# Performance work log

Measured on AMD Instinct MI355X. Metric: run time of the kernel, lower is better.

The kernel has to match this reference:

```python
import jax, jax.numpy as jnp
import numpy as np
from jax.ops import segment_sum

N_NODES = 50000
N_EDGES = 800000
IN_CH = 128
HID = 256
N_CLASSES = 10
N_GRAPHS = 64


def setup_inputs() -> dict:
    key = jax.random.key(0)
    ks = jax.random.split(key, 12)
    x = jax.random.normal(ks[0], (N_NODES, IN_CH), dtype=jnp.float32)
    edge_index = jax.random.randint(ks[1], (2, N_EDGES), 0, N_NODES, dtype=jnp.int64)
    batch = jnp.sort(jax.random.randint(ks[2], (N_NODES,), 0, N_GRAPHS, dtype=jnp.int64))
    def glorot(k, shape):
        lim = (6.0 / (shape[0] + shape[1])) ** 0.5
        return jax.random.uniform(k, shape, jnp.float32, -lim, lim)
    # GraphConv has two linear maps: lin_rel (neighbor aggregate, with bias) and lin_root (self)
    params = {
        "W1_root": glorot(ks[3], (IN_CH, HID)),  "W1_nbr": glorot(ks[4], (IN_CH, HID)),  "b1": jnp.zeros((HID,), jnp.float32),
        "W2_root": glorot(ks[5], (HID, HID)),    "W2_nbr": glorot(ks[6], (HID, HID)),    "b2": jnp.zeros((HID,), jnp.float32),
        "W3_root": glorot(ks[7], (HID, HID)),    "W3_nbr": glorot(ks[8], (HID, HID)),    "b3": jnp.zeros((HID,), jnp.float32),
        "W_lin": glorot(ks[9], (HID, N_CLASSES)), "b_lin": jnp.zeros((N_CLASSES,), jnp.float32),
    }
    return {"x": x, "edge_index": edge_index, "batch": batch, **params}


def _graph_conv(x, src, dst, W_root, W_nbr, b):
    # out_i = W_root x_i + W_nbr * sum_{j: (j->i) in E} x_j + b   (PyG GraphConv, aggr='add')
    agg = segment_sum(x[src], dst, num_segments=N_NODES)  # [N, d]
    return x @ W_root + agg @ W_nbr + b


def reference(x, edge_index, batch,
              W1_root, W1_nbr, b1,
              W2_root, W2_nbr, b2,
              W3_root, W3_nbr, b3,
              W_lin, b_lin):
    src, dst = edge_index[0], edge_index[1]
    h = jax.nn.relu(_graph_conv(x, src, dst, W1_root, W1_nbr, b1))
    h = jax.nn.relu(_graph_conv(h, src, dst, W2_root, W2_nbr, b2))
    h = _graph_conv(h, src, dst, W3_root, W3_nbr, b3)
    # global_mean_pool over graph ids
    sums = segment_sum(h, batch, num_segments=N_GRAPHS)                        # [G, HID]
    counts = segment_sum(jnp.ones((h.shape[0],), h.dtype), batch, num_segments=N_GRAPHS)
    pooled = sums / jnp.maximum(counts, 1.0)[:, None]
    # dropout is identity at inference
    return pooled @ W_lin + b_lin  # [G, n_classes]
```

## Files before the change

### kernel.cpp

```cpp
#include <hip/hip_runtime.h>
#include <stdint.h>

#define N_NODES 50000
#define N_EDGES 800000
#define IN_CH 128
#define HID 256
#define N_GRAPHS 64
#define N_CLASSES 10

#define FUSED_WG ((N_NODES + 63) / 64)
#define NB ((N_NODES + 127) / 128)
#define EPB 4096
#define CAP 4096

typedef unsigned short u16;
typedef __attribute__((ext_vector_type(8))) short short8;
typedef __attribute__((ext_vector_type(4))) float f32x4;

__device__ __forceinline__ float bf2f(uint32_t u) {
    union { uint32_t i; float f; } v; v.i = u << 16; return v.f;
}
__device__ __forceinline__ uint32_t f2bf(float f) {
    union { float f; uint32_t i; } v; v.f = f;
    return (v.i + 0x7FFFu + ((v.i >> 16) & 1u)) >> 16;
}

__global__ void __launch_bounds__(512) bin_pass(const int* __restrict__ src,
                                                const int* __restrict__ dst,
                                                int* __restrict__ gcnt,
                                                uint32_t* __restrict__ tmp)
{
    __shared__ int hist[NB];
    __shared__ int base[NB];
    int t = threadIdx.x;
    for (int i = t; i < NB; i += 512) hist[i] = 0;
    __syncthreads();
    const int e0 = blockIdx.x * EPB;
    int b_[8], s_[8], d_[8];
    #pragma unroll
    for (int k = 0; k < 8; ++k) {
        int e = e0 + k * 512 + t;
        if (e < N_EDGES) {
            int d = dst[e];
            b_[k] = d >> 7;
            d_[k] = d & 127;
            s_[k] = src[e];
            atomicAdd(&hist[b_[k]], 1);
        } else b_[k] = -1;
    }
    __syncthreads();
    for (int i = t; i < NB; i += 512) {
        int c = hist[i];
        base[i] = c ? atomicAdd(&gcnt[i], c) : 0;
        hist[i] = 0;
    }
    __syncthreads();
    #pragma unroll
    for (int k = 0; k < 8; ++k) {
        if (b_[k] >= 0) {
            int r = atomicAdd(&hist[b_[k]], 1);
            int pos = base[b_[k]] + r;
            if (pos < CAP)
                tmp[(size_t)b_[k] * CAP + pos] = ((uint32_t)s_[k] << 7) | (uint32_t)d_[k];
        }
    }
}

__global__ void __launch_bounds__(512) bucket_scan(const int* __restrict__ gcnt,
                                                   int* __restrict__ boff,
                                                   int* __restrict__ row_start)
{
    __shared__ int buf[512];
    int t = threadIdx.x;
    int v = (t < NB) ? gcnt[t] : 0;
    buf[t] = v;
    __syncthreads();
    #pragma unroll
    for (int off = 1; off < 512; off <<= 1) {
        int a = (t >= off) ? buf[t - off] : 0;
        __syncthreads();
        buf[t] += a;
        __syncthreads();
    }
    if (t < NB) boff[t] = buf[t] - v;
    if (t == 0) row_start[N_NODES] = N_EDGES;
}

__global__ void __launch_bounds__(256) debin2(const uint32_t* __restrict__ tmp,
                                              const int* __restrict__ gcnt,
                                              const int* __restrict__ boff,
                                              int* __restrict__ row_start,
                                              int* __restrict__ esrc)
{
    __shared__ int h[128];
    __shared__ int pre[128];
    __shared__ int cur[128];
    const int b = blockIdx.x;
    const int n0 = b * 128;
    const int nn = min(128, N_NODES - n0);
    const int t = threadIdx.x;
    const int cnt = min(gcnt[b], CAP);
    const int bb = boff[b];
    const uint32_t* te = tmp + (size_t)b * CAP;

    if (t < 128) h[t] = 0;
    __syncthreads();
    for (int p = t; p < cnt; p += 256)
        atomicAdd(&h[te[p] & 127u], 1);
    __syncthreads();
    if (t < 128) pre[t] = h[t];
    __syncthreads();
    #pragma unroll
    for (int off = 1; off < 128; off <<= 1) {
        int a = (t >= off && t < 128) ? pre[t - off] : 0;
        __syncthreads();
        if (t < 128) pre[t] += a;
        __syncthreads();
    }
    if (t < nn) {
        int rs = bb + pre[t] - h[t];
        row_start[n0 + t] = rs;
        cur[t] = rs;
    }
    __syncthreads();
    for (int p = t; p < cnt; p += 256) {
        uint32_t v = te[p];
        int pos = atomicAdd(&cur[v & 127u], 1);
        esrc[pos] = (int)(v >> 7);
    }
}

#define XB 3125
__global__ void __launch_bounds__(256)
cvt_all(const float* __restrict__ x, u16* __restrict__ xb,
        const float* __restrict__ W1r, const float* __restrict__ W1n,
        const float* __restrict__ W2r, const float* __restrict__ W2n,
        const float* __restrict__ W3r, const float* __restrict__ W3n,
        u16* __restrict__ o1r, u16* __restrict__ o1n,
        u16* __restrict__ o2r, u16* __restrict__ o2n,
        u16* __restrict__ o3r, u16* __restrict__ o3n)
{
    if (blockIdx.x < XB) {
        int id = blockIdx.x * 256 + threadIdx.x;
        const float4 a = *reinterpret_cast<const float4*>(x + (size_t)id * 8);
        const float4 b = *reinterpret_cast<const float4*>(x + (size_t)id * 8 + 4);
        uint4 o;
        o.x = f2bf(a.x) | (f2bf(a.y) << 16);
        o.y = f2bf(a.z) | (f2bf(a.w) << 16);
        o.z = f2bf(b.x) | (f2bf(b.y) << 16);
        o.w = f2bf(b.z) | (f2bf(b.w) << 16);
        *reinterpret_cast<uint4*>(xb + (size_t)id * 8) = o;
        return;
    }
    int id = (blockIdx.x - XB) * 256 + threadIdx.x;
    if (id < 65536) {
        int m = id >> 15;
        int r = id & 32767;
        int k = r >> 8, n = r & 255;
        const float* W = m ? W1n : W1r;
        u16* O = m ? o1n : o1r;
        O[n * 128 + k] = (u16)f2bf(W[r]);
    } else {
        id -= 65536;
        int m = id >> 16;
        int r = id & 65535;
        int k = r >> 8, n = r & 255;
        const float* W = (m == 0) ? W2r : (m == 1) ? W2n : (m == 2) ? W3r : W3n;
        u16* O = (m == 0) ? o2r : (m == 1) ? o2n : (m == 2) ? o3r : o3n;
        O[n * 256 + k] = (u16)f2bf(W[r]);
    }
}

template<int RELU, int K>
__global__ void __launch_bounds__(512, 4)
fused_layer(const u16* __restrict__ feat,
            const int* __restrict__ row_start,
            const int* __restrict__ esrc,
            const u16* __restrict__ B1t,
            const u16* __restrict__ B2t,
            const float* __restrict__ bias,
            u16* __restrict__ C,
            int M)
{
    __shared__ __align__(16) u16 agg[64][K + 8];
    __shared__ __align__(16) u16 As[64][40];
    __shared__ __align__(16) u16 Bs[256][40];

    const int orig = blockIdx.x;
    const int q = FUSED_WG / 8, r = FUSED_WG % 8;
    const int xcd = orig % 8;
    const int wg = (xcd < r ? xcd * (q + 1) : r * (q + 1) + (xcd - r) * q) + orig / 8;

    const int tid = threadIdx.x;
    const int bm = wg * 64;

    {
        constexpr int NCH = K / 2;
        constexpr int LPN = NCH / 8;
        constexpr int NPP = 512 / LPN;
        constexpr int PASSES = 64 / NPP;
        const int lane = tid % LPN;
        const int nl0  = tid / LPN;

        for (int h = 0; h < 2; ++h) {
            const u16* fp = feat + h * NCH + lane * 8;
            #pragma unroll
            for (int p = 0; p < PASSES; ++p) {
                const int nl = p * NPP + nl0;
                const int node = bm + nl;
                float acc[8] = {0.f, 0.f, 0.f, 0.f, 0.f, 0.f, 0.f, 0.f};
                if (node < M) {
                    const int s = row_start[node], e = row_start[node + 1];
                    auto add = [&](uint4 v) {
                        acc[0] += bf2f(v.x & 0xFFFF); acc[1] += bf2f(v.x >> 16);
                        acc[2] += bf2f(v.y & 0xFFFF); acc[3] += bf2f(v.y >> 16);
                        acc[4] += bf2f(v.z & 0xFFFF); acc[5] += bf2f(v.z >> 16);
                        acc[6] += bf2f(v.w & 0xFFFF); acc[7] += bf2f(v.w >> 16);
                    };
                    int j = s;
                    for (; j + 3 < e; j += 4) {
                        int s0 = esrc[j], s1 = esrc[j + 1], s2 = esrc[j + 2], s3 = esrc[j + 3];
                        uint4 v0 = *reinterpret_cast<const uint4*>(fp + (size_t)s0 * K);
                        uint4 v1 = *reinterpret_cast<const uint4*>(fp + (size_t)s1 * K);
                        uint4 v2 = *reinterpret_cast<const uint4*>(fp + (size_t)s2 * K);
                        uint4 v3 = *reinterpret_cast<const uint4*>(fp + (size_t)s3 * K);
                        add(v0); add(v1); add(v2); add(v3);
                    }
                    for (; j < e; ++j)
                        add(*reinterpret_cast<const uint4*>(fp + (size_t)esrc[j] * K));
                }
                uint4 o;
                o.x = f2bf(acc[0]) | (f2bf(acc[1]) << 16);
                o.y = f2bf(acc[2]) | (f2bf(acc[3]) << 16);
                o.z = f2bf(acc[4]) | (f2bf(acc[5]) << 16);
                o.w = f2bf(acc[6]) | (f2bf(acc[7]) << 16);
                *reinterpret_cast<uint4*>(&agg[nl][h * NCH + lane * 8]) = o;
            }
        }
    }
    __syncthreads();

    const int w  = tid >> 6;
    const int wm = (w >> 2) * 32;
    const int wn = (w & 3) * 64;
    const int l  = tid & 63;
    const int lr = l & 15;
    const int kb = (l >> 4) * 8;

    f32x4 acc[2][4];
    #pragma unroll
    for (int i = 0; i < 2; ++i)
        #pragma unroll
        for (int j = 0; j < 4; ++j)
            acc[i][j] = (f32x4){0.f, 0.f, 0.f, 0.f};

    const int row_a = tid >> 2;
    const int c8    = (tid & 3) * 8;

    for (int k0 = 0; k0 < K; k0 += 32) {
        if (tid < 256) {
            uint4 va = make_uint4(0u, 0u, 0u, 0u);
            int gr = bm + row_a;
            if (gr < M)
                va = *reinterpret_cast<const uint4*>(feat + (size_t)gr * K + k0 + c8);
            *reinterpret_cast<uint4*>(&As[row_a][c8]) = va;
        }
        #pragma unroll
        for (int it = 0; it < 2; ++it) {
            int row = (tid >> 2) + it * 128;
            uint4 vb = *reinterpret_cast<const uint4*>(B1t + (size_t)row * K + k0 + c8);
            *reinterpret_cast<uint4*>(&Bs[row][c8]) = vb;
        }
        __syncthreads();
        short8 af[2], bfr[4];
        #pragma unroll
        for (int f = 0; f < 2; ++f)
            af[f] = *reinterpret_cast<const short8*>(&As[wm + f * 16 + lr][kb]);
        #pragma unroll
        for (int f = 0; f < 4; ++f)
            bfr[f] = *reinterpret_cast<const short8*>(&Bs[wn + f * 16 + lr][kb]);
        #pragma unroll
        for (int fm = 0; fm < 2; ++fm)
            #pragma unroll
            for (int fn = 0; fn < 4; ++fn)
                acc[fm][fn] = __builtin_amdgcn_mfma_f32_16x16x32_bf16(
                    af[fm], bfr[fn], acc[fm][fn], 0, 0, 0);
        __syncthreads();
    }

    for (int k0 = 0; k0 < K; k0 += 32) {
        #pragma unroll
        for (int it = 0; it < 2; ++it) {
            int row = (tid >> 2) + it * 128;
            uint4 vb = *reinterpret_cast<const uint4*>(B2t + (size_t)row * K + k0 + c8);
            *reinterpret_cast<uint4*>(&Bs[row][c8]) = vb;
        }
        __syncthreads();
        short8 af[2], bfr[4];
        #pragma unroll
        for (int f = 0; f < 2; ++f)
            af[f] = *reinterpret_cast<const short8*>(&agg[wm + f * 16 + lr][k0 + kb]);
        #pragma unroll
        for (int f = 0; f < 4; ++f)
            bfr[f] = *reinterpret_cast<const short8*>(&Bs[wn + f * 16 + lr][kb]);
        #pragma unroll
        for (int fm = 0; fm < 2; ++fm)
            #pragma unroll
            for (int fn = 0; fn < 4; ++fn)
                acc[fm][fn] = __builtin_amdgcn_mfma_f32_16x16x32_bf16(
                    af[fm], bfr[fn], acc[fm][fn], 0, 0, 0);
        __syncthreads();
    }

    const int r4 = (l >> 4) * 4;
    #pragma unroll
    for (int fm = 0; fm < 2; ++fm) {
        #pragma unroll
        for (int rr = 0; rr < 4; ++rr) {
            int row = bm + wm + fm * 16 + r4 + rr;
            if (row >= M) continue;
            #pragma unroll
            for (int fn = 0; fn < 4; ++fn) {
                int col = wn + fn * 16 + lr;
                float v = acc[fm][fn][rr] + bias[col];
                if (RELU) v = fmaxf(v, 0.f);
                C[(size_t)row * HID + col] = (u16)f2bf(v);
            }
        }
    }
}

__device__ __forceinline__ int lower_bound_g(const int* __restrict__ batch, int g)
{
    int lo = 0, hi = N_NODES;
    while (lo < hi) {
        int mid = (lo + hi) >> 1;
        if (batch[mid] < g) lo = mid + 1; else hi = mid;
    }
    return lo;
}

__global__ void pool1_kernel(const u16* __restrict__ h, const int* __restrict__ batch,
                             float* __restrict__ partial)
{
    int g = blockIdx.x >> 3;
    int c = blockIdx.x & 7;
    int t = threadIdx.x;
    int s = lower_bound_g(batch, g);
    int e = lower_bound_g(batch, g + 1);
    int cnt = e - s;
    int a = s + (int)(((long long)cnt * c) >> 3);
    int b = s + (int)(((long long)cnt * (c + 1)) >> 3);
    float acc = 0.f;
    for (int i = a; i < b; ++i)
        acc += bf2f(h[(size_t)i * HID + t]);
    partial[(size_t)blockIdx.x * HID + t] = acc;
}

__global__ void pool2_final(const float* __restrict__ partial, const int* __restrict__ batch,
                            const float* __restrict__ W_lin, const float* __restrict__ b_lin,
                            float* __restrict__ out)
{
    __shared__ float v[HID];
    int g = blockIdx.x;
    int t = threadIdx.x;
    float acc = 0.f;
    #pragma unroll
    for (int c = 0; c < 8; ++c)
        acc += partial[(size_t)(g * 8 + c) * HID + t];
    float cnt = fmaxf((float)(lower_bound_g(batch, g + 1) - lower_bound_g(batch, g)), 1.f);
    v[t] = acc / cnt;
    __syncthreads();
    if (t < N_CLASSES) {
        float s = b_lin[t];
        for (int k = 0; k < HID; ++k)
            s += v[k] * W_lin[k * N_CLASSES + t];
        out[g * N_CLASSES + t] = s;
    }
}

extern "C" void kernel_launch(void* const* d_in, const int* in_sizes, int n_in,
                              void* d_out, int out_size, void* d_ws, size_t ws_size,
                              hipStream_t stream)
{
    const float* x     = (const float*)d_in[0];
    const int*   ei    = (const int*)d_in[1];
    const int*   batch = (const int*)d_in[2];
    const float* W1r = (const float*)d_in[3];
    const float* W1n = (const float*)d_in[4];
    const float* b1  = (const float*)d_in[5];
    const float* W2r = (const float*)d_in[6];
    const float* W2n = (const float*)d_in[7];
    const float* b2  = (const float*)d_in[8];
    const float* W3r = (const float*)d_in[9];
    const float* W3n = (const float*)d_in[10];
    const float* b3  = (const float*)d_in[11];
    const float* Wl  = (const float*)d_in[12];
    const float* bl  = (const float*)d_in[13];
    float* out = (float*)d_out;

    const int* src = ei;
    const int* dst = ei + N_EDGES;

    char* base = (char*)d_ws;
    size_t off = 0;
    auto alloc = [&](size_t bytes) { char* p = base + off; off += (bytes + 255) & ~(size_t)255; return p; };
    u16* x_bf = (u16*)alloc((size_t)N_NODES * IN_CH * 2);
    u16* hA   = (u16*)alloc((size_t)N_NODES * HID * 2);
    u16* hB   = (u16*)alloc((size_t)N_NODES * HID * 2);
    u16* wt1r = (u16*)alloc((size_t)HID * IN_CH * 2);
    u16* wt1n = (u16*)alloc((size_t)HID * IN_CH * 2);
    u16* wt2r = (u16*)alloc((size_t)HID * HID * 2);
    u16* wt2n = (u16*)alloc((size_t)HID * HID * 2);
    u16* wt3r = (u16*)alloc((size_t)HID * HID * 2);
    u16* wt3n = (u16*)alloc((size_t)HID * HID * 2);
    float* partial = (float*)alloc((size_t)N_GRAPHS * 8 * HID * 4);
    int* row_start = (int*)alloc((size_t)(N_NODES + 1) * 4);
    int* esrc      = (int*)alloc((size_t)N_EDGES * 4);
    uint32_t* tmp  = (uint32_t*)alloc((size_t)NB * CAP * 4);
    int* gcnt      = (int*)alloc((size_t)NB * 4);
    int* boff      = (int*)alloc((size_t)NB * 4);

    hipMemsetAsync(gcnt, 0, NB * sizeof(int), stream);
    bin_pass<<<(N_EDGES + EPB - 1) / EPB, 512, 0, stream>>>(src, dst, gcnt, tmp);
    bucket_scan<<<1, 512, 0, stream>>>(gcnt, boff, row_start);
    debin2<<<NB, 256, 0, stream>>>(tmp, gcnt, boff, row_start, esrc);

    cvt_all<<<XB + 1280, 256, 0, stream>>>(x, x_bf, W1r, W1n, W2r, W2n, W3r, W3n,
                                           wt1r, wt1n, wt2r, wt2n, wt3r, wt3n);

    fused_layer<1, IN_CH><<<FUSED_WG, 512, 0, stream>>>(x_bf, row_start, esrc,
                                                        wt1r, wt1n, b1, hA, N_NODES);
    fused_layer<1, HID><<<FUSED_WG, 512, 0, stream>>>(hA, row_start, esrc,
                                                      wt2r, wt2n, b2, hB, N_NODES);
    fused_layer<0, HID><<<FUSED_WG, 512, 0, stream>>>(hB, row_start, esrc,
                                                      wt3r, wt3n, b3, hA, N_NODES);

    pool1_kernel<<<N_GRAPHS * 8, HID, 0, stream>>>(hA, batch, partial);
    pool2_final<<<N_GRAPHS, HID, 0, stream>>>(partial, batch, Wl, bl, out);
}
```

Before: 329.3 us.

## Halve aggregation LDS buffer by interleaving half-width gather with neighbor GEMM

Restructures the fused GraphConv layer so the root GEMM runs first and neighbor aggregation is done in two column halves, each immediately consumed by its slice of the neighbor GEMM. This halves the shared-memory agg buffer, and the launch bound is raised from 4 to 6 blocks per CU to exploit the lower LDS footprint and hide gather latency. The risk is tighter register limits under the higher occupancy bound, which could cause spills, plus an extra barrier per half.

```diff
diff --git a/kernel.cpp b/kernel.cpp
--- a/kernel.cpp
+++ b/kernel.cpp
@@ -172,7 +172,7 @@
 }
 
 template<int RELU, int K>
-__global__ void __launch_bounds__(512, 4)
+__global__ void __launch_bounds__(512, 6)
 fused_layer(const u16* __restrict__ feat,
             const int* __restrict__ row_start,
             const int* __restrict__ esrc,
@@ -182,7 +182,8 @@
             u16* __restrict__ C,
             int M)
 {
-    __shared__ __align__(16) u16 agg[64][K + 8];
+    constexpr int HALF = K / 2;
+    __shared__ __align__(16) u16 agg[64][HALF + 4];
     __shared__ __align__(16) u16 As[64][40];
     __shared__ __align__(16) u16 Bs[256][40];
 
@@ -194,28 +195,74 @@
     const int tid = threadIdx.x;
     const int bm = wg * 64;
 
-    {
-        constexpr int NCH = K / 2;
-        constexpr int LPN = NCH / 8;
-        constexpr int NPP = 512 / LPN;
-        constexpr int PASSES = 64 / NPP;
-        const int lane = tid % LPN;
-        const int nl0  = tid / LPN;
-
-        for (int h = 0; h < 2; ++h) {
-            const u16* fp = feat + h * NCH + lane * 8;
+    const int w  = tid >> 6;
+    const int wm = (w >> 2) * 32;
+    const int wn = (w & 3) * 64;
+    const int l  = tid & 63;
+    const int lr = l & 15;
+    const int kb = (l >> 4) * 8;
+    const int c8 = (tid & 3) * 8;
+    const int row_b = tid >> 2;
+
+    f32x4 acc[2][4];
+    #pragma unroll
+    for (int i = 0; i < 2; ++i)
+        #pragma unroll
+        for (int j = 0; j < 4; ++j)
+            acc[i][j] = (f32x4){0.f, 0.f, 0.f, 0.f};
+
+    for (int k0 = 0; k0 < K; k0 += 32) {
+        if (tid < 256) {
+            uint4 va = make_uint4(0u, 0u, 0u, 0u);
+            int gr = bm + row_b;
+            if (gr < M)
+                va = *reinterpret_cast<const uint4*>(feat + (size_t)gr * K + k0 + c8);
+            *reinterpret_cast<uint4*>(&As[row_b][c8]) = va;
+        }
+        #pragma unroll
+        for (int it = 0; it < 2; ++it) {
+            int row = row_b + it * 128;
+            uint4 vb = *reinterpret_cast<const uint4*>(B1t + (size_t)row * K + k0 + c8);
+            *reinterpret_cast<uint4*>(&Bs[row][c8]) = vb;
+        }
+        __syncthreads();
+        short8 af[2], bfr[4];
+        #pragma unroll
+        for (int f = 0; f < 2; ++f)
+            af[f] = *reinterpret_cast<const short8*>(&As[wm + f * 16 + lr][kb]);
+        #pragma unroll
+        for (int f = 0; f < 4; ++f)
+            bfr[f] = *reinterpret_cast<const short8*>(&Bs[wn + f * 16 + lr][kb]);
+        #pragma unroll
+        for (int fm = 0; fm < 2; ++fm)
+            #pragma unroll
+            for (int fn = 0; fn < 4; ++fn)
+                acc[fm][fn] = __builtin_amdgcn_mfma_f32_16x16x32_bf16(
+                    af[fm], bfr[fn], acc[fm][fn], 0, 0, 0);
+        __syncthreads();
+    }
+
+    #pragma unroll
+    for (int h = 0; h < 2; ++h) {
+        {
+            constexpr int LPN = HALF / 8;
+            constexpr int NPP = 512 / LPN;
+            constexpr int PASSES = 64 / NPP;
+            const int lane = tid % LPN;
+            const int nl0  = tid / LPN;
+            const u16* fp = feat + h * HALF + lane * 8;
             #pragma unroll
             for (int p = 0; p < PASSES; ++p) {
                 const int nl = p * NPP + nl0;
                 const int node = bm + nl;
-                float acc[8] = {0.f, 0.f, 0.f, 0.f, 0.f, 0.f, 0.f, 0.f};
+                float a8[8] = {0.f, 0.f, 0.f, 0.f, 0.f, 0.f, 0.f, 0.f};
                 if (node < M) {
                     const int s = row_start[node], e = row_start[node + 1];
                     auto add = [&](uint4 v) {
-                        acc[0] += bf2f(v.x & 0xFFFF); acc[1] += bf2f(v.x >> 16);
-                        acc[2] += bf2f(v.y & 0xFFFF); acc[3] += bf2f(v.y >> 16);
-                        acc[4] += bf2f(v.z & 0xFFFF); acc[5] += bf2f(v.z >> 16);
-                        acc[6] += bf2f(v.w & 0xFFFF); acc[7] += bf2f(v.w >> 16);
+                        a8[0] += bf2f(v.x & 0xFFFF); a8[1] += bf2f(v.x >> 16);
+                        a8[2] += bf2f(v.y & 0xFFFF); a8[3] += bf2f(v.y >> 16);
+                        a8[4] += bf2f(v.z & 0xFFFF); a8[5] += bf2f(v.z >> 16);
+                        a8[6] += bf2f(v.w & 0xFFFF); a8[7] += bf2f(v.w >> 16);
                     };
                     int j = s;
                     for (; j + 3 < e; j += 4) {
@@ -230,86 +277,39 @@
                         add(*reinterpret_cast<const uint4*>(fp + (size_t)esrc[j] * K));
                 }
                 uint4 o;
-                o.x = f2bf(acc[0]) | (f2bf(acc[1]) << 16);
-                o.y = f2bf(acc[2]) | (f2bf(acc[3]) << 16);
-                o.z = f2bf(acc[4]) | (f2bf(acc[5]) << 16);
-                o.w = f2bf(acc[6]) | (f2bf(acc[7]) << 16);
-                *reinterpret_cast<uint4*>(&agg[nl][h * NCH + lane * 8]) = o;
+                o.x = f2bf(a8[0]) | (f2bf(a8[1]) << 16);
+                o.y = f2bf(a8[2]) | (f2bf(a8[3]) << 16);
+                o.z = f2bf(a8[4]) | (f2bf(a8[5]) << 16);
+                o.w = f2bf(a8[6]) | (f2bf(a8[7]) << 16);
+                *reinterpret_cast<uint4*>(&agg[nl][lane * 8]) = o;
             }
         }
-    }
-    __syncthreads();
-
-    const int w  = tid >> 6;
-    const int wm = (w >> 2) * 32;
-    const int wn = (w & 3) * 64;
-    const int l  = tid & 63;
-    const int lr = l & 15;
-    const int kb = (l >> 4) * 8;
-
-    f32x4 acc[2][4];
-    #pragma unroll
-    for (int i = 0; i < 2; ++i)
-        #pragma unroll
-        for (int j = 0; j < 4; ++j)
-            acc[i][j] = (f32x4){0.f, 0.f, 0.f, 0.f};
-
-    const int row_a = tid >> 2;
-    const int c8    = (tid & 3) * 8;
-
-    for (int k0 = 0; k0 < K; k0 += 32) {
-        if (tid < 256) {
-            uint4 va = make_uint4(0u, 0u, 0u, 0u);
-            int gr = bm + row_a;
-            if (gr < M)
-                va = *reinterpret_cast<const uint4*>(feat + (size_t)gr * K + k0 + c8);
-            *reinterpret_cast<uint4*>(&As[row_a][c8]) = va;
-        }
-        #pragma unroll
-        for (int it = 0; it < 2; ++it) {
-            int row = (tid >> 2) + it * 128;
-            uint4 vb = *reinterpret_cast<const uint4*>(B1t + (size_t)row * K + k0 + c8);
-            *reinterpret_cast<uint4*>(&Bs[row][c8]) = vb;
-        }
-        __syncthreads();
-        short8 af[2], bfr[4];
-        #pragma unroll
-        for (int f = 0; f < 2; ++f)
-            af[f] = *reinterpret_cast<const short8*>(&As[wm + f * 16 + lr][kb]);
-        #pragma unroll
-        for (int f = 0; f < 4; ++f)
-            bfr[f] = *reinterpret_cast<const short8*>(&Bs[wn + f * 16 + lr][kb]);
-        #pragma unroll
-        for (int fm = 0; fm < 2; ++fm)
-            #pragma unroll
-            for (int fn = 0; fn < 4; ++fn)
-                acc[fm][fn] = __builtin_amdgcn_mfma_f32_16x16x32_bf16(
-                    af[fm], bfr[fn], acc[fm][fn], 0, 0, 0);
-        __syncthreads();
-    }
-
-    for (int k0 = 0; k0 < K; k0 += 32) {
-        #pragma unroll
-        for (int it = 0; it < 2; ++it) {
-            int row = (tid >> 2) + it * 128;
-            uint4 vb = *reinterpret_cast<const uint4*>(B2t + (size_t)row * K + k0 + c8);
-            *reinterpret_cast<uint4*>(&Bs[row][c8]) = vb;
-        }
-        __syncthreads();
-        short8 af[2], bfr[4];
-        #pragma unroll
-        for (int f = 0; f < 2; ++f)
-            af[f] = *reinterpret_cast<const short8*>(&agg[wm + f * 16 + lr][k0 + kb]);
-        #pragma unroll
-        for (int f = 0; f < 4; ++f)
-            bfr[f] = *reinterpret_cast<const short8*>(&Bs[wn + f * 16 + lr][kb]);
-        #pragma unroll
-        for (int fm = 0; fm < 2; ++fm)
-            #pragma unroll
-            for (int fn = 0; fn < 4; ++fn)
-                acc[fm][fn] = __builtin_amdgcn_mfma_f32_16x16x32_bf16(
-                    af[fm], bfr[fn], acc[fm][fn], 0, 0, 0);
-        __syncthreads();
+        __syncthreads();
+
+        for (int k0l = 0; k0l < HALF; k0l += 32) {
+            #pragma unroll
+            for (int it = 0; it < 2; ++it) {
+                int row = row_b + it * 128;
+                uint4 vb = *reinterpret_cast<const uint4*>(
+                    B2t + (size_t)row * K + h * HALF + k0l + c8);
+                *reinterpret_cast<uint4*>(&Bs[row][c8]) = vb;
+            }
+            __syncthreads();
+            short8 af[2], bfr[4];
+            #pragma unroll
+            for (int f = 0; f < 2; ++f)
+                af[f] = *reinterpret_cast<const short8*>(&agg[wm + f * 16 + lr][k0l + kb]);
+            #pragma unroll
+            for (int f = 0; f < 4; ++f)
+                bfr[f] = *reinterpret_cast<const short8*>(&Bs[wn + f * 16 + lr][kb]);
+            #pragma unroll
+            for (int fm = 0; fm < 2; ++fm)
+                #pragma unroll
+                for (int fn = 0; fn < 4; ++fn)
+                    acc[fm][fn] = __builtin_amdgcn_mfma_f32_16x16x32_bf16(
+                        af[fm], bfr[fn], acc[fm][fn], 0, 0, 0);
+            __syncthreads();
+        }
     }
 
     const int r4 = (l >> 4) * 4;
```

New measurement: 376.9 us. +14.4%, slower.
